# Kernel tuning notes

Measured on AMD Instinct MI355X. Metric: run time of the kernel, lower is better.

## Reference

```python
import jax, jax.numpy as jnp
import numpy as np

B, C, N = 8, 256, 3072
BN_EPS = 1e-5


def setup_inputs() -> dict:
    key = jax.random.key(0)
    ks = jax.random.split(key, 8)
    s = 1.0 / np.sqrt(C)
    return {
        "x": jax.random.normal(ks[0], (B, C, N), dtype=jnp.float32),
        "q": jax.random.normal(ks[1], (B, C, N), dtype=jnp.float32),
        "Wq": jax.random.normal(ks[2], (C, C), dtype=jnp.float32) * s,
        "Wk": jax.random.normal(ks[3], (C, C), dtype=jnp.float32) * s,
        "Wv": jax.random.normal(ks[4], (C, C), dtype=jnp.float32) * s,
        "bv": jax.random.normal(ks[5], (C,), dtype=jnp.float32) * 0.01,
        "Wt": jax.random.normal(ks[6], (C, C), dtype=jnp.float32) * s,
        "bt": jax.random.normal(ks[7], (C,), dtype=jnp.float32) * 0.01,
        "gamma": jnp.ones((C,), dtype=jnp.float32),
        "beta": jnp.zeros((C,), dtype=jnp.float32),
    }


def reference(x, q, Wq, Wk, Wv, bv, Wt, bt, gamma, beta):
    # 1x1 conv projections (Conv1d(C,C,1) == per-point matmul)
    x_q = jnp.einsum('oc,bcn->bno', Wq, q)            # [B, N, C]
    x_k = jnp.einsum('oc,bcn->bon', Wk, x)            # [B, C, N]
    x_v = jnp.einsum('oc,bcn->bno', Wv, x) + bv       # [B, N, C]

    energy = jnp.einsum('bnc,bcm->bnm', x_q, x_k)     # [B, N, N]
    attention = jax.nn.softmax(energy, axis=-1)       # row softmax
    # extra L1 re-normalization over columns (dim=1)
    attention = attention / (1e-9 + attention.sum(axis=1, keepdims=True))

    x_r = jnp.einsum('bnm,bmc->bcn', attention, x_v)  # [B, C, N]

    # trans_conv(q - x_r) with bias
    t = jnp.einsum('oc,bcn->bon', Wt, q - x_r) + bt[None, :, None]

    # BatchNorm1d (training mode: batch stats over B and N, biased var)
    mean = t.mean(axis=(0, 2), keepdims=True)
    var = ((t - mean) ** 2).mean(axis=(0, 2), keepdims=True)
    h = (t - mean) / jnp.sqrt(var + BN_EPS)
    h = h * gamma[None, :, None] + beta[None, :, None]

    return q + jax.nn.relu(h)
```

## Files before the change

kernel.cpp:

```cpp
#include <hip/hip_runtime.h>

#define BB 8
#define CC 256
#define NN 3072

typedef unsigned short u16;
typedef unsigned int   u32;
typedef __attribute__((ext_vector_type(8))) __bf16 bf16x8;
typedef __attribute__((ext_vector_type(8))) u16    u16x8;
typedef __attribute__((ext_vector_type(4))) float  f32x4;

__device__ __forceinline__ float bf2f(u16 u){ u32 x=(u32)u<<16; return __builtin_bit_cast(float,x); }
__device__ __forceinline__ u16 f2bf(float f){ u32 i=__builtin_bit_cast(u32,f); i += 0x7FFFu + ((i>>16)&1u); return (u16)(i>>16); }
__device__ __forceinline__ u32 fkey(float f){ u32 u=__builtin_bit_cast(u32,f); return (u&0x80000000u)? ~u : (u|0x80000000u); }
__device__ __forceinline__ float funkey(u32 k){ u32 u=(k&0x80000000u)? (k^0x80000000u) : ~k; return __builtin_bit_cast(float,u); }

__device__ __forceinline__ void gl_lds16(const u16* g, u16* l){
  __builtin_amdgcn_global_load_lds((const __attribute__((address_space(1))) void*)g,
                                   (__attribute__((address_space(3))) void*)l, 16, 0, 0);
}

__global__ void prep_w(const float* __restrict__ Wq, const float* __restrict__ Wk,
                       const float* __restrict__ Wv, const float* __restrict__ Wt,
                       u16* __restrict__ WarrQ, u16* __restrict__ WarrK,
                       u16* __restrict__ WarrV, u16* __restrict__ WtH){
  int idx = blockIdx.x*256 + threadIdx.x;
  int p = idx >> 16; int oc = idx & 65535; int o = oc >> 8; int c = oc & 255;
  const float* W = (p==0)?Wq:(p==1)?Wk:(p==2)?Wv:Wt;
  float v = W[oc];
  if(p==0) v *= 1.4426950408889634f;
  u16 hi = f2bf(v);
  if(p==3){ WtH[oc]=hi; return; }
  u16 lo = f2bf(v - bf2f(hi));
  u16* dst = (p==0)?WarrQ:(p==1)?WarrK:WarrV;
  dst[(size_t)o*768 + c] = hi; dst[(size_t)o*768 + 256 + c] = hi; dst[(size_t)o*768 + 512 + c] = lo;
}

__global__ void prep_x(const float* __restrict__ x, const float* __restrict__ q,
                       u16* __restrict__ xs, u16* __restrict__ qs){
  int z=blockIdx.z, b=z&7, src=z>>3;
  const float* in = src? q : x;
  u16* outp = src? qs : xs;
  int n0=blockIdx.x*64, c0=blockIdx.y*64;
  __shared__ float t[64][65];
  int tid=threadIdx.x;
  {
    int r=tid>>2, nr=(tid&3)*16;
    const float* base = in + ((size_t)b*CC + c0 + r)*NN + n0 + nr;
    #pragma unroll
    for(int j=0;j<16;j+=4){
      f32x4 v = *(const f32x4*)(base + j);
      t[r][nr+j]=v[0]; t[r][nr+j+1]=v[1]; t[r][nr+j+2]=v[2]; t[r][nr+j+3]=v[3];
    }
  }
  __syncthreads();
  {
    int n=tid>>2, cw=(tid&3)*16;
    u16 hb[16] __attribute__((aligned(16)));
    u16 lb[16] __attribute__((aligned(16)));
    #pragma unroll
    for(int j=0;j<16;j++){
      float v=t[cw+j][n];
      u16 h=f2bf(v); hb[j]=h; lb[j]=f2bf(v-bf2f(h));
    }
    u16* ob = outp + ((size_t)b*NN + n0 + n)*512 + c0 + cw;
    *(u16x8*)(ob)       = *(const u16x8*)(hb);
    *(u16x8*)(ob+8)     = *(const u16x8*)(hb+8);
    *(u16x8*)(ob+256)   = *(const u16x8*)(lb);
    *(u16x8*)(ob+264)   = *(const u16x8*)(lb+8);
  }
}

template<int AMAP,int BMAP,int EPI,int KTT>
__global__ __launch_bounds__(256,2)
void gemm_k(const u16* __restrict__ A, const u16* __restrict__ BT,
            int lda,int ldbt,long long sA,long long sB,int KT,
            u16* __restrict__ dst, long long sD, int lddst,
            float* __restrict__ dstF,
            const float* __restrict__ bias,
            const float* __restrict__ recl,
            u32* __restrict__ rmax,
            float* __restrict__ rsum,
            float* __restrict__ S1, float* __restrict__ S2,
            const float* __restrict__ qsrc)
{
  __shared__ u16 sm[33024] __attribute__((aligned(16)));
  float* smax = (float*)(sm + 32768);
  const int tid=threadIdx.x, lane=tid&63, wave=tid>>6, wr=wave>>1, wc=wave&1;
  const int nt=blockIdx.x, mt=blockIdx.y, b=blockIdx.z;
  const int lr = lane>>4, lc = lane&15;

  if constexpr (EPI==3){ if(tid<128) smax[tid] = funkey(rmax[(size_t)b*NN + mt*128 + tid]); }

  f32x4 acc[4][4];
  #pragma unroll
  for(int i=0;i<4;i++){
    #pragma unroll
    for(int j=0;j<4;j++){ acc[i][j][0]=0.f; acc[i][j][1]=0.f; acc[i][j][2]=0.f; acc[i][j][3]=0.f; }
  }

  const u16* Ab = A + (size_t)b*sA + (size_t)mt*128*lda;
  const u16* Bb = BT + (size_t)b*sB + (size_t)nt*128*ldbt;

  const u16* Ap[4]; const u16* Bp[4];
  #pragma unroll
  for(int i=0;i<4;i++){
    int f=i*256+tid, row=f>>3, gc=(f&7)^(row&7);
    Ap[i] = Ab + (size_t)row*lda  + gc*8;
    Bp[i] = Bb + (size_t)row*ldbt + gc*8;
  }

  auto stage=[&](int p,int ao,int bo){
    #pragma unroll
    for(int i=0;i<4;i++) gl_lds16(Ap[i]+ao, sm + p*16384 + (i*256 + wave*64)*8);
    #pragma unroll
    for(int i=0;i<4;i++) gl_lds16(Bp[i]+bo, sm + p*16384 + 8192 + (i*256 + wave*64)*8);
  };
  auto aoff=[&](int kt)->int{ int g=kt>>2,t4=(kt&3)*64;
    return t4 + (AMAP==0? g*256 : (AMAP==1? (g==2?256:0) : (g==1?256:0))); };
  auto boff=[&](int kt)->int{ int g=kt>>2,t4=(kt&3)*64;
    return t4 + (BMAP==0? g*256 : (BMAP==1? (g==2?256:0) : (g==1?256:0))); };
  auto compute=[&](int p){
    const u16* As = sm + p*16384;
    const u16* Bs = As + 8192;
    #pragma unroll
    for(int kk=0;kk<2;kk++){
      bf16x8 af[4], bfv[4];
      int c0 = kk*4 + lr;
      #pragma unroll
      for(int i=0;i<4;i++){
        int row = wr*64 + i*16 + lc;
        af[i]  = *(const bf16x8*)(As + (size_t)row*64 + ((c0^(row&7))*8));
      }
      #pragma unroll
      for(int j=0;j<4;j++){
        int row = wc*64 + j*16 + lc;
        bfv[j] = *(const bf16x8*)(Bs + (size_t)row*64 + ((c0^(row&7))*8));
      }
      #pragma unroll
      for(int i=0;i<4;i++){
        #pragma unroll
        for(int j=0;j<4;j++)
          acc[i][j] = __builtin_amdgcn_mfma_f32_16x16x32_bf16(af[i], bfv[j], acc[i][j], 0,0,0);
      }
    }
  };

  if constexpr (KTT>0){
    stage(0, aoff(0), boff(0));
    #pragma unroll
    for(int kt=0;kt<KTT;kt++){
      if(kt+1<KTT){
        stage((kt+1)&1, aoff(kt+1), boff(kt+1));
        asm volatile("s_waitcnt vmcnt(8)" ::: "memory");
      } else {
        asm volatile("s_waitcnt vmcnt(0)" ::: "memory");
      }
      __syncthreads();
      compute(kt&1);
      __syncthreads();
    }
  } else {
    stage(0, 0, 0);
    int ao = 64;
    for(int kt=0;kt<KT;kt++){
      if(kt+1<KT){
        stage((kt+1)&1, ao, ao);
        asm volatile("s_waitcnt vmcnt(8)" ::: "memory");
        ao += 64;
      } else {
        asm volatile("s_waitcnt vmcnt(0)" ::: "memory");
      }
      __syncthreads();
      compute(kt&1);
      __syncthreads();
    }
  }

  const int rbase = mt*128 + wr*64;
  const int cbase = nt*128 + wc*64;

  if constexpr (EPI==0){
    u16* D = dst + (size_t)b*sD;
    #pragma unroll
    for(int i=0;i<4;i++){
      #pragma unroll
      for(int j=0;j<4;j++){
        int col = cbase + j*16 + lc;
        #pragma unroll
        for(int r=0;r<4;r++){
          int row = rbase + i*16 + lr*4 + r;
          float v = acc[i][j][r];
          u16 h = f2bf(v); u16 lo = f2bf(v - bf2f(h));
          D[(size_t)row*lddst + col] = h;
          D[(size_t)row*lddst + 256 + col] = lo;
        }
      }
    }
  } else if constexpr (EPI==1){
    u16* D = dst + (size_t)b*sD;
    #pragma unroll
    for(int i=0;i<4;i++){
      #pragma unroll
      for(int r=0;r<4;r++){
        int row = rbase + i*16 + lr*4 + r;
        float bv_ = bias[row];
        #pragma unroll
        for(int j=0;j<4;j++){
          int col = cbase + j*16 + lc;
          D[(size_t)row*lddst + col] = f2bf(acc[i][j][r] + bv_);
        }
      }
    }
  } else if constexpr (EPI==2){
    #pragma unroll
    for(int i=0;i<4;i++){
      #pragma unroll
      for(int r=0;r<4;r++){
        float mx = acc[i][0][r];
        mx = fmaxf(mx, acc[i][1][r]); mx = fmaxf(mx, acc[i][2][r]); mx = fmaxf(mx, acc[i][3][r]);
        mx = fmaxf(mx, __shfl_xor(mx,1));
        mx = fmaxf(mx, __shfl_xor(mx,2));
        mx = fmaxf(mx, __shfl_xor(mx,4));
        mx = fmaxf(mx, __shfl_xor(mx,8));
        if(lc==0){
          int row = rbase + i*16 + lr*4 + r;
          atomicMax(&rmax[(size_t)b*NN + row], fkey(mx));
        }
      }
    }
  } else if constexpr (EPI==3){
    __syncthreads();
    u16* Pb = sm;
    #pragma unroll
    for(int i=0;i<4;i++){
      #pragma unroll
      for(int r=0;r<4;r++){
        int rl = wr*64 + i*16 + lr*4 + r;
        float mx = smax[rl];
        float s=0.f;
        #pragma unroll
        for(int j=0;j<4;j++){
          float e2 = acc[i][j][r] - mx;
          float p;
          asm("v_exp_f32 %0, %1" : "=v"(p) : "v"(e2));
          s+=p;
          Pb[rl*136 + wc*64 + j*16 + lc] = f2bf(p);
        }
        s += __shfl_xor(s,1); s += __shfl_xor(s,2); s += __shfl_xor(s,4); s += __shfl_xor(s,8);
        if(lc==0) atomicAdd(&rsum[(size_t)b*NN + mt*128 + rl], s);
      }
    }
    __syncthreads();
    u16* D = dst + (size_t)b*sD;
    #pragma unroll
    for(int it=0; it<8; ++it){
      int ch = it*256 + tid, row = ch>>4, ccol=(ch&15)*8;
      *(u16x8*)(D + (size_t)(mt*128+row)*lddst + nt*128 + ccol) = *(const u16x8*)(Pb + row*136 + ccol);
    }
  } else if constexpr (EPI==4){
    const float* rl_ = recl + (size_t)b*NN;
    const float* qb  = qsrc + (size_t)b*CC*NN;
    u16* D = dst + (size_t)b*sD;
    #pragma unroll
    for(int i=0;i<4;i++){
      int nb = rbase + i*16 + lr*4;
      float rc[4];
      #pragma unroll
      for(int r=0;r<4;r++) rc[r] = rl_[nb+r];
      #pragma unroll
      for(int j=0;j<4;j++){
        int c_ = cbase + j*16 + lc;
        f32x4 qv = *(const f32x4*)(qb + (size_t)c_*NN + nb);
        #pragma unroll
        for(int r=0;r<4;r++){
          float dq = qv[r] - acc[i][j][r]*rc[r];
          D[(size_t)(nb+r)*lddst + c_] = f2bf(dq);
        }
      }
    }
  } else if constexpr (EPI==5){
    float* Df = dstF + (size_t)b*CC*NN;
    #pragma unroll
    for(int i=0;i<4;i++){
      #pragma unroll
      for(int r=0;r<4;r++){
        int row = rbase + i*16 + lr*4 + r;
        float bt_ = bias[row];
        float s=0.f, s2=0.f;
        #pragma unroll
        for(int j=0;j<4;j++){
          int col = cbase + j*16 + lc;
          float v = acc[i][j][r] + bt_;
          Df[(size_t)row*NN + col] = v;
          s += v; s2 += v*v;
        }
        s  += __shfl_xor(s,1);  s  += __shfl_xor(s,2);  s  += __shfl_xor(s,4);  s  += __shfl_xor(s,8);
        s2 += __shfl_xor(s2,1); s2 += __shfl_xor(s2,2); s2 += __shfl_xor(s2,4); s2 += __shfl_xor(s2,8);
        if(lc==0){ atomicAdd(&S1[row], s); atomicAdd(&S2[row], s2); }
      }
    }
  }
}

__global__ void recl_k(const float* __restrict__ l, float* __restrict__ recl){
  int i = blockIdx.x*256 + threadIdx.x;
  recl[i] = 1.0f / l[i];
}

__global__ void colsum_k(const u16* __restrict__ P, const float* __restrict__ recl,
                         float* __restrict__ colsum){
  int b = blockIdx.z;
  int m0 = blockIdx.x*1024 + threadIdx.x*8;
  int n0 = blockIdx.y*48;
  const u16* Pb = P + (size_t)b*NN*NN;
  const float* rb = recl + (size_t)b*NN;
  float acc[8] = {0,0,0,0,0,0,0,0};
  for(int i=0;i<48;i++){
    int n = n0+i;
    u16x8 v = *(const u16x8*)(Pb + (size_t)n*NN + m0);
    float r = rb[n];
    #pragma unroll
    for(int j=0;j<8;j++) acc[j] += bf2f(v[j]) * r;
  }
  float* cb = colsum + (size_t)b*NN + m0;
  #pragma unroll
  for(int j=0;j<8;j++) atomicAdd(&cb[j], acc[j]);
}

__global__ void vprime_k(const u16* __restrict__ XV, const float* __restrict__ colsum,
                         u16* __restrict__ VpT){
  size_t base = ((size_t)blockIdx.x*256 + threadIdx.x)*8;
  int m = (int)(base % NN);
  int b = (int)(base / ((size_t)NN*CC));
  const float* cs = colsum + (size_t)b*NN + m;
  u16x8 v = *(const u16x8*)(XV + base);
  u16x8 o;
  #pragma unroll
  for(int j=0;j<8;j++) o[j] = f2bf(bf2f(v[j]) / (1e-9f + cs[j]));
  *(u16x8*)(VpT + base) = o;
}

__global__ void bnfin_k(const float* __restrict__ S1, const float* __restrict__ S2,
                        const float* __restrict__ gamma, const float* __restrict__ beta,
                        float* __restrict__ scale, float* __restrict__ shift){
  int c = threadIdx.x;
  float cnt = (float)(BB*NN);
  float mean = S1[c]/cnt;
  float var  = S2[c]/cnt - mean*mean;
  float rs = rsqrtf(var + 1e-5f);
  float sc = gamma[c]*rs;
  scale[c] = sc;
  shift[c] = beta[c] - mean*sc;
}

__global__ void outk(const float* __restrict__ T, const float* __restrict__ q,
                     const float* __restrict__ scale, const float* __restrict__ shift,
                     float* __restrict__ out){
  size_t i4 = (size_t)blockIdx.x*256 + threadIdx.x;
  int c = (int)((i4 / 768) & 255);
  f32x4 tv = *(const f32x4*)(T + i4*4);
  f32x4 qv = *(const f32x4*)(q + i4*4);
  float sc = scale[c], sh = shift[c];
  f32x4 o;
  #pragma unroll
  for(int k=0;k<4;k++){
    float h = tv[k]*sc + sh;
    o[k] = qv[k] + (h>0.f? h : 0.f);
  }
  *(f32x4*)(out + i4*4) = o;
}

extern "C" void kernel_launch(void* const* d_in, const int* in_sizes, int n_in,
                              void* d_out, int out_size, void* d_ws, size_t ws_size,
                              hipStream_t stream)
{
  const float* x  = (const float*)d_in[0];
  const float* q  = (const float*)d_in[1];
  const float* Wq = (const float*)d_in[2];
  const float* Wk = (const float*)d_in[3];
  const float* Wv = (const float*)d_in[4];
  const float* bv = (const float*)d_in[5];
  const float* Wt = (const float*)d_in[6];
  const float* bt = (const float*)d_in[7];
  const float* gamma=(const float*)d_in[8];
  const float* beta =(const float*)d_in[9];
  float* out = (float*)d_out;
  char* ws = (char*)d_ws;

  u16* P    = (u16*)(ws + 0);
  u16* XQ   = (u16*)(ws + 150994944);
  u16* XK   = (u16*)(ws + 176160768);
  u16* QS   = (u16*)(ws + 201326592);
  u16* XS   = (u16*)(ws + 226492416);
  u16* XV   = (u16*)(ws + 251658240);
  u16* WarrQ= (u16*)(ws + 264241152);
  u16* WarrK= (u16*)(ws + 264634368);
  u16* WarrV= (u16*)(ws + 265027584);
  u16* WtH  = (u16*)(ws + 265420800);
  u32* rmax = (u32*)(ws + 265551872);
  float* l  = (float*)(ws + 265551872 + 98304);
  float* colsum=(float*)(ws + 265551872 + 196608);
  float* S1 = (float*)(ws + 265551872 + 294912);
  float* S2 = (float*)(ws + 265551872 + 295936);
  float* recl = (float*)(ws + 265848832);
  float* scale= (float*)(ws + 265947136);
  float* shift= (float*)(ws + 265948160);
  u16* VpT = XQ;
  float* T = (float*)QS;
  u16* DQ  = XS;

  hipMemsetAsync(ws + 265551872, 0, 296960, stream);

  prep_w<<<1024,256,0,stream>>>(Wq,Wk,Wv,Wt,WarrQ,WarrK,WarrV,WtH);
  prep_x<<<dim3(48,4,16),256,0,stream>>>(x,q,XS,QS);

  gemm_k<2,0,0,12><<<dim3(2,24,8),256,0,stream>>>(QS, WarrQ, 512, 768, (long long)NN*512, 0, 12,
      XQ, (long long)NN*512, 512, nullptr, nullptr, nullptr, nullptr, nullptr, nullptr, nullptr, nullptr);
  gemm_k<2,0,0,12><<<dim3(2,24,8),256,0,stream>>>(XS, WarrK, 512, 768, (long long)NN*512, 0, 12,
      XK, (long long)NN*512, 512, nullptr, nullptr, nullptr, nullptr, nullptr, nullptr, nullptr, nullptr);
  gemm_k<0,2,1,12><<<dim3(24,2,8),256,0,stream>>>(WarrV, XS, 768, 512, 0, (long long)NN*512, 12,
      XV, (long long)CC*NN, NN, nullptr, bv, nullptr, nullptr, nullptr, nullptr, nullptr, nullptr);
  gemm_k<0,0,2,4><<<dim3(6,24,8),256,0,stream>>>(XQ, XK, 512, 512, (long long)NN*512, (long long)NN*512, 4,
      nullptr, 0, 0, nullptr, nullptr, nullptr, rmax, nullptr, nullptr, nullptr, nullptr);
  gemm_k<1,2,3,12><<<dim3(24,24,8),256,0,stream>>>(XQ, XK, 512, 512, (long long)NN*512, (long long)NN*512, 12,
      P, (long long)NN*NN, NN, nullptr, nullptr, nullptr, rmax, l, nullptr, nullptr, nullptr);
  recl_k<<<96,256,0,stream>>>(l, recl);
  colsum_k<<<dim3(3,64,8),128,0,stream>>>(P, recl, colsum);
  vprime_k<<<3072,256,0,stream>>>(XV, colsum, VpT);
  gemm_k<0,0,4,0><<<dim3(2,24,8),256,0,stream>>>(P, VpT, NN, NN, (long long)NN*NN, (long long)CC*NN, 48,
      DQ, (long long)NN*CC, CC, nullptr, nullptr, recl, nullptr, nullptr, nullptr, nullptr, q);
  gemm_k<0,0,5,4><<<dim3(24,2,8),256,0,stream>>>(WtH, DQ, 256, 256, 0, (long long)NN*CC, 4,
      nullptr, 0, 0, T, bt, nullptr, nullptr, nullptr, S1, S2, nullptr);
  bnfin_k<<<1,256,0,stream>>>(S1,S2,gamma,beta,scale,shift);
  outk<<<6144,256,0,stream>>>(T,q,scale,shift,out);
}
```

Baseline: 571.2 us.

## Single-buffer GEMM LDS to raise occupancy, stage EPI0 stores, read split-bf16 q

Switches the GEMM mainloop from double-buffered async LDS staging to a single buffer. This halves shared memory, and the launch bounds now allow four blocks per CU instead of two. The trade is that the load-compute overlap within a block is gone, and there is an extra barrier per k-step. The EPI0 hi/lo bf16 output now goes through LDS for coalesced 16-byte stores, and EPI4 reads q from the pre-split hi/lo bf16 copy instead of strided fp32. That changes q's precision slightly and could tighten the register budget.

```diff
diff --git a/kernel.cpp b/kernel.cpp
--- a/kernel.cpp
+++ b/kernel.cpp
@@ -72,7 +72,7 @@
 }
 
 template<int AMAP,int BMAP,int EPI,int KTT>
-__global__ __launch_bounds__(256,2)
+__global__ __launch_bounds__(256,4)
 void gemm_k(const u16* __restrict__ A, const u16* __restrict__ BT,
             int lda,int ldbt,long long sA,long long sB,int KT,
             u16* __restrict__ dst, long long sD, int lddst,
@@ -84,8 +84,9 @@
             float* __restrict__ S1, float* __restrict__ S2,
             const float* __restrict__ qsrc)
 {
-  __shared__ u16 sm[33024] __attribute__((aligned(16)));
-  float* smax = (float*)(sm + 32768);
+  __shared__ u16 sm[17664] __attribute__((aligned(16)));
+  u16* As = sm; u16* Bs = sm + 8192;
+  float* smax = (float*)(sm + 17408);
   const int tid=threadIdx.x, lane=tid&63, wave=tid>>6, wr=wave>>1, wc=wave&1;
   const int nt=blockIdx.x, mt=blockIdx.y, b=blockIdx.z;
   const int lr = lane>>4, lc = lane&15;
@@ -110,19 +111,17 @@
     Bp[i] = Bb + (size_t)row*ldbt + gc*8;
   }
 
-  auto stage=[&](int p,int ao,int bo){
-    #pragma unroll
-    for(int i=0;i<4;i++) gl_lds16(Ap[i]+ao, sm + p*16384 + (i*256 + wave*64)*8);
-    #pragma unroll
-    for(int i=0;i<4;i++) gl_lds16(Bp[i]+bo, sm + p*16384 + 8192 + (i*256 + wave*64)*8);
+  auto stage=[&](int ao,int bo){
+    #pragma unroll
+    for(int i=0;i<4;i++) gl_lds16(Ap[i]+ao, As + (i*256 + wave*64)*8);
+    #pragma unroll
+    for(int i=0;i<4;i++) gl_lds16(Bp[i]+bo, Bs + (i*256 + wave*64)*8);
   };
   auto aoff=[&](int kt)->int{ int g=kt>>2,t4=(kt&3)*64;
     return t4 + (AMAP==0? g*256 : (AMAP==1? (g==2?256:0) : (g==1?256:0))); };
   auto boff=[&](int kt)->int{ int g=kt>>2,t4=(kt&3)*64;
     return t4 + (BMAP==0? g*256 : (BMAP==1? (g==2?256:0) : (g==1?256:0))); };
-  auto compute=[&](int p){
-    const u16* As = sm + p*16384;
-    const u16* Bs = As + 8192;
+  auto compute=[&](){
     #pragma unroll
     for(int kk=0;kk<2;kk++){
       bf16x8 af[4], bfv[4];
@@ -147,33 +146,23 @@
   };
 
   if constexpr (KTT>0){
-    stage(0, aoff(0), boff(0));
     #pragma unroll
     for(int kt=0;kt<KTT;kt++){
-      if(kt+1<KTT){
-        stage((kt+1)&1, aoff(kt+1), boff(kt+1));
-        asm volatile("s_waitcnt vmcnt(8)" ::: "memory");
-      } else {
-        asm volatile("s_waitcnt vmcnt(0)" ::: "memory");
-      }
+      if(kt) __syncthreads();
+      stage(aoff(kt), boff(kt));
+      asm volatile("s_waitcnt vmcnt(0)" ::: "memory");
       __syncthreads();
-      compute(kt&1);
+      compute();
+    }
+  } else {
+    int ao = 0;
+    for(int kt=0;kt<KT;kt++){
+      if(kt) __syncthreads();
+      stage(ao, ao);
+      asm volatile("s_waitcnt vmcnt(0)" ::: "memory");
       __syncthreads();
-    }
-  } else {
-    stage(0, 0, 0);
-    int ao = 64;
-    for(int kt=0;kt<KT;kt++){
-      if(kt+1<KT){
-        stage((kt+1)&1, ao, ao);
-        asm volatile("s_waitcnt vmcnt(8)" ::: "memory");
-        ao += 64;
-      } else {
-        asm volatile("s_waitcnt vmcnt(0)" ::: "memory");
-      }
-      __syncthreads();
-      compute(kt&1);
-      __syncthreads();
+      compute();
+      ao += 64;
     }
   }
 
@@ -182,19 +171,29 @@
 
   if constexpr (EPI==0){
     u16* D = dst + (size_t)b*sD;
-    #pragma unroll
-    for(int i=0;i<4;i++){
-      #pragma unroll
-      for(int j=0;j<4;j++){
-        int col = cbase + j*16 + lc;
+    u16* Pb = sm;
+    #pragma unroll
+    for(int half=0; half<2; ++half){
+      __syncthreads();
+      #pragma unroll
+      for(int i=0;i<4;i++){
         #pragma unroll
         for(int r=0;r<4;r++){
-          int row = rbase + i*16 + lr*4 + r;
-          float v = acc[i][j][r];
-          u16 h = f2bf(v); u16 lo = f2bf(v - bf2f(h));
-          D[(size_t)row*lddst + col] = h;
-          D[(size_t)row*lddst + 256 + col] = lo;
-        }
+          int rl = wr*64 + i*16 + lr*4 + r;
+          #pragma unroll
+          for(int j=0;j<4;j++){
+            float v = acc[i][j][r];
+            u16 h = f2bf(v);
+            Pb[rl*136 + wc*64 + j*16 + lc] = half ? f2bf(v - bf2f(h)) : h;
+          }
+        }
+      }
+      __syncthreads();
+      #pragma unroll
+      for(int it=0; it<8; ++it){
+        int ch = it*256 + tid, row = ch>>4, ccol=(ch&15)*8;
+        *(u16x8*)(D + (size_t)(mt*128+row)*lddst + half*256 + nt*128 + ccol)
+            = *(const u16x8*)(Pb + row*136 + ccol);
       }
     }
   } else if constexpr (EPI==1){
@@ -260,7 +259,7 @@
     }
   } else if constexpr (EPI==4){
     const float* rl_ = recl + (size_t)b*NN;
-    const float* qb  = qsrc + (size_t)b*CC*NN;
+    const u16* qs_b  = (const u16*)qsrc + (size_t)b*NN*512;
     u16* D = dst + (size_t)b*sD;
     #pragma unroll
     for(int i=0;i<4;i++){
@@ -271,10 +270,11 @@
       #pragma unroll
       for(int j=0;j<4;j++){
         int c_ = cbase + j*16 + lc;
-        f32x4 qv = *(const f32x4*)(qb + (size_t)c_*NN + nb);
         #pragma unroll
         for(int r=0;r<4;r++){
-          float dq = qv[r] - acc[i][j][r]*rc[r];
+          const u16* qr = qs_b + (size_t)(nb+r)*512 + c_;
+          float qv = bf2f(qr[0]) + bf2f(qr[256]);
+          float dq = qv - acc[i][j][r]*rc[r];
           D[(size_t)(nb+r)*lddst + c_] = f2bf(dq);
         }
       }
@@ -429,7 +429,7 @@
   colsum_k<<<dim3(3,64,8),128,0,stream>>>(P, recl, colsum);
   vprime_k<<<3072,256,0,stream>>>(XV, colsum, VpT);
   gemm_k<0,0,4,0><<<dim3(2,24,8),256,0,stream>>>(P, VpT, NN, NN, (long long)NN*NN, (long long)CC*NN, 48,
-      DQ, (long long)NN*CC, CC, nullptr, nullptr, recl, nullptr, nullptr, nullptr, nullptr, q);
+      DQ, (long long)NN*CC, CC, nullptr, nullptr, recl, nullptr, nullptr, nullptr, nullptr, (const float*)QS);
   gemm_k<0,0,5,4><<<dim3(24,2,8),256,0,stream>>>(WtH, DQ, 256, 256, 0, (long long)NN*CC, 4,
       nullptr, 0, 0, T, bt, nullptr, nullptr, nullptr, S1, S2, nullptr);
   bnfin_k<<<1,256,0,stream>>>(S1,S2,gamma,beta,scale,shift);
```

New measurement: 669.6 us. +17.2%, slower.
